# Optimization experiments

Measured on AMD Instinct MI355X. Metric: run time of the kernel, lower is better.

Reference implementation:

```python
import jax, jax.numpy as jnp
import numpy as np

B, S, D = 2, 2048, 1024
H, DK, DV = 16, 64, 64

def setup_inputs() -> dict:
    key = jax.random.key(0)
    ks = jax.random.split(key, 16)
    sc = 0.02
    inp = {
        'Q': jax.random.normal(ks[0], (B, S, D), jnp.float32),
        'K': jax.random.normal(ks[1], (B, S, D), jnp.float32),
        'V': jax.random.normal(ks[2], (B, S, D), jnp.float32),
        'attn_mask': jax.random.randint(ks[3], (B, S, S), 0, 2) > 0,
        'wq': jax.random.normal(ks[4], (H * DK, D), jnp.float32) * sc,
        'bq': jnp.zeros((H * DK,), jnp.float32),
        'wk': jax.random.normal(ks[5], (H * DK, D), jnp.float32) * sc,
        'bk': jnp.zeros((H * DK,), jnp.float32),
        'wv': jax.random.normal(ks[6], (H * DV, D), jnp.float32) * sc,
        'bv': jnp.zeros((H * DV,), jnp.float32),
        'wo': jax.random.normal(ks[7], (D, H * DV), jnp.float32) * sc,
        'bo': jnp.zeros((D,), jnp.float32),
        'gamma': jnp.ones((D,), jnp.float32),
        'beta': jnp.zeros((D,), jnp.float32),
    }
    return inp

def reference(Q, K, V, attn_mask, wq, bq, wk, bk, wv, bv, wo, bo, gamma, beta):
    b = Q.shape[0]
    # Faithful to torch: .view(B, H, -1, dk) with NO transpose (reshape-based head split)
    q = (Q @ wq.T + bq).reshape(b, H, -1, DK)
    k = (K @ wk.T + bk).reshape(b, H, -1, DK)
    v = (V @ wv.T + bv).reshape(b, H, -1, DV)
    scores = jnp.einsum('bhqd,bhkd->bhqk', q, k) / np.sqrt(DK).astype(np.float32)
    scores = jnp.where(attn_mask[:, None, :, :], jnp.float32(-1e9), scores)
    attn = jax.nn.softmax(scores, axis=-1)
    context = jnp.einsum('bhqk,bhkd->bhqd', attn, v)  # [B,H,S,dv]
    context = context.transpose(0, 2, 1, 3).reshape(b, -1, H * DV)
    output = context @ wo.T + bo
    x = output + Q
    mu = jnp.mean(x, axis=-1, keepdims=True)
    var = jnp.var(x, axis=-1, keepdims=True)
    return (x - mu) / jnp.sqrt(var + 1e-5) * gamma + beta
```

## Files before the change

### kernel.cpp

```cpp
#include <hip/hip_runtime.h>
#include <hip/hip_bf16.h>
#include <stdint.h>

typedef __bf16 bf16_t;
typedef __bf16 bf16x8 __attribute__((ext_vector_type(8)));
typedef __bf16 bf16x4 __attribute__((ext_vector_type(4)));
typedef float  f32x4  __attribute__((ext_vector_type(4)));

#if __has_builtin(__builtin_amdgcn_exp2f)
#define EXP2F __builtin_amdgcn_exp2f
#else
#define EXP2F exp2f
#endif


__device__ __forceinline__ void async_copy16(void* lds, const void* gptr) {
  __builtin_amdgcn_global_load_lds(
      (const __attribute__((address_space(1))) void*)gptr,
      (__attribute__((address_space(3))) void*)lds, 16, 0, 0);
}

__device__ __forceinline__ f32x4 splat4(float x) {
  f32x4 r; r[0] = x; r[1] = x; r[2] = x; r[3] = x; return r;
}

__device__ __forceinline__ uint32_t pack_bf16(float lo, float hi) {
  const uint32_t l = (uint32_t)__builtin_bit_cast(unsigned short, (bf16_t)lo);
  const uint32_t h = (uint32_t)__builtin_bit_cast(unsigned short, (bf16_t)hi);
  return (h << 16) | l;
}

__device__ __forceinline__ bool detect_fp32(const void* p) {
  const uint16_t* h = (const uint16_t*)p;
  int weird_even = 0, zero_even = 0, nz_odd = 0;
  for (int i = 0; i < 32; ++i) {
    uint16_t e = h[2 * i], o = h[2 * i + 1];
    int ee = (e >> 7) & 0xFF;
    if (e == 0) zero_even++;
    else if (ee < 90 || ee > 160) weird_even++;
    if (o != 0) nz_odd++;
  }
  return (weird_even >= 6) || (zero_even == 32 && nz_odd >= 1);
}

__global__ __launch_bounds__(256) void convert_all(
    const void* s0, const void* s1, const void* s2, const void* s3,
    const void* s4, const void* s5, const void* s6, const void* s7,
    const void* s8, const void* s9, const void* s10, const void* s11,
    const void* s12, char* __restrict__ ws) {
  const void* srcs[13] = {s0, s1, s2, s3, s4, s5, s6, s7, s8, s9, s10, s11, s12};
  const int counts[13] = {4194304, 4194304, 4194304,
                          1048576, 1024, 1048576, 1024,
                          1048576, 1024, 1048576, 1024,
                          1024, 1024};
  const size_t dofs[13] = {
      0ull, 8ull << 20, 16ull << 20,
      24ull << 20, (32ull << 20) + 0 * 8192, 26ull << 20, (32ull << 20) + 1 * 8192,
      28ull << 20, (32ull << 20) + 2 * 8192, 30ull << 20, (32ull << 20) + 3 * 8192,
      (32ull << 20) + 4 * 8192, (32ull << 20) + 5 * 8192};
  const int bi = blockIdx.y;
  const void* src = srcs[bi];
  bf16x8* dst = (bf16x8*)(ws + dofs[bi]);
  const int nv = counts[bi] >> 3;
  const bool f32 = detect_fp32(src);
  const int idx = blockIdx.x * 256 + threadIdx.x;
  const int stride = gridDim.x * 256;
  if (f32) {
    const float4* s4p = (const float4*)src;
    for (int i = idx; i < nv; i += stride) {
      float4 a = s4p[2 * i], b = s4p[2 * i + 1];
      bf16x8 o;
      o[0] = (bf16_t)a.x; o[1] = (bf16_t)a.y; o[2] = (bf16_t)a.z; o[3] = (bf16_t)a.w;
      o[4] = (bf16_t)b.x; o[5] = (bf16_t)b.y; o[6] = (bf16_t)b.z; o[7] = (bf16_t)b.w;
      dst[i] = o;
    }
  } else {
    const bf16x8* s8p = (const bf16x8*)src;
    for (int i = idx; i < nv; i += stride) dst[i] = s8p[i];
  }
}

__device__ __forceinline__ int detect_mask(const uint8_t* p) {
  const uint32_t* w = (const uint32_t*)p;
  bool i32 = true;
  for (int i = 0; i < 32; ++i) i32 &= (w[i] <= 1u);
  if (i32) return 0;
  const uint16_t* hh = (const uint16_t*)p;
  bool evz = true, oddok = true, allbf = true, allf16 = true;
  for (int i = 0; i < 32; ++i) {
    uint16_t e = hh[2 * i], o = hh[2 * i + 1];
    evz &= (e == 0);
    oddok &= (o == 0 || o == 0x3F80);
    allbf &= (e == 0 || e == 0x3F80) && (o == 0 || o == 0x3F80);
    allf16 &= (e == 0 || e == 0x3C00) && (o == 0 || o == 0x3C00);
  }
  if (evz && oddok) return 1;
  if (allbf || allf16) return 2;
  return 3;
}

__global__ __launch_bounds__(256) void mask_pack(const uint8_t* __restrict__ mraw,
                                                 uint8_t* __restrict__ outp) {
  const int mode = detect_mask(mraw);
  const int bq = blockIdx.x;
  const int L = threadIdx.x;
  uint32_t byte = 0;
  if (mode <= 1) {
    const uint4* m = (const uint4*)mraw;
    const size_t b4 = (size_t)bq * 512 + L * 2;
    uint4 a = m[b4], c = m[b4 + 1];
    byte = (a.x != 0u ? 1u : 0u) | (a.y != 0u ? 2u : 0u) |
           (a.z != 0u ? 4u : 0u) | (a.w != 0u ? 8u : 0u) |
           (c.x != 0u ? 16u : 0u) | (c.y != 0u ? 32u : 0u) |
           (c.z != 0u ? 64u : 0u) | (c.w != 0u ? 128u : 0u);
  } else if (mode == 2) {
    const uint16_t* m = (const uint16_t*)mraw;
    const size_t base = (size_t)bq * 2048 + L * 8;
    for (int j = 0; j < 8; ++j) byte |= (m[base + j] != 0 ? 1u : 0u) << j;
  } else {
    const size_t base = (size_t)bq * 2048 + L * 8;
    for (int j = 0; j < 8; ++j) byte |= (mraw[base + j] != 0 ? 1u : 0u) << j;
  }
  outp[(size_t)bq * 256 + L] = (uint8_t)byte;
}

template <int MODE, int BM>
__device__ __forceinline__ void gemm_tile(const bf16_t* __restrict__ X,
                                          const bf16_t* __restrict__ W,
                                          const bf16_t* __restrict__ bias,
                                          const float* __restrict__ QresF,
                                          const bf16_t* __restrict__ QresB,
                                          bool qres_is_f32,
                                          void* __restrict__ outv) {
  __shared__ __align__(16) bf16_t sA[BM * 32];
  __shared__ __align__(16) bf16_t sB[128 * 32];
  const int tm = blockIdx.x * BM;
  const int tn = blockIdx.y * 128;
  const int t = threadIdx.x;
  const int w = t >> 6, l = t & 63, lc = l & 15, ql = l >> 4;
  const int wm = (BM == 128) ? (w >> 1) * 64 : 0;
  const int wn = (BM == 128) ? (w & 1) * 64 : w * 32;
  const int NJ = (BM == 128) ? 4 : 2;
  f32x4 acc[4][(BM == 128) ? 4 : 2];
  for (int i = 0; i < 4; ++i)
    for (int j = 0; j < NJ; ++j) acc[i][j] = splat4(0.0f);

  const int m0 = t >> 2;
  const int kc0 = (t & 3) * 8;

  for (int k0 = 0; k0 < 1024; k0 += 32) {
    __syncthreads();
    async_copy16((char*)sA + w * 1024, X + (size_t)(tm + m0) * 1024 + k0 + kc0);
    if (BM == 128)
      async_copy16((char*)sA + 4096 + w * 1024,
                   X + (size_t)(tm + 64 + m0) * 1024 + k0 + kc0);
    async_copy16((char*)sB + w * 1024,        W + (size_t)(tn + m0) * 1024 + k0 + kc0);
    async_copy16((char*)sB + 4096 + w * 1024, W + (size_t)(tn + 64 + m0) * 1024 + k0 + kc0);
    __syncthreads();

    bf16x8 af[4], bfr[(BM == 128) ? 4 : 2];
    for (int i = 0; i < 4; ++i)
      af[i] = *(const bf16x8*)(sA + (wm + i * 16 + lc) * 32 + ql * 8);
    for (int j = 0; j < NJ; ++j)
      bfr[j] = *(const bf16x8*)(sB + (wn + j * 16 + lc) * 32 + ql * 8);
    for (int i = 0; i < 4; ++i)
      for (int j = 0; j < NJ; ++j)
        acc[i][j] = __builtin_amdgcn_mfma_f32_16x16x32_bf16(af[i], bfr[j], acc[i][j], 0, 0, 0);
  }

  float bvals[(BM == 128) ? 4 : 2];
  for (int j = 0; j < NJ; ++j) bvals[j] = (float)bias[tn + wn + j * 16 + lc];
  for (int i = 0; i < 4; ++i) {
    for (int j = 0; j < NJ; ++j) {
      const int col = tn + wn + j * 16 + lc;
      for (int v = 0; v < 4; ++v) {
        const int row = tm + wm + i * 16 + ql * 4 + v;
        float val = acc[i][j][v] + bvals[j];
        if (MODE == 0) {
          ((bf16_t*)outv)[(size_t)row * 1024 + col] = (bf16_t)val;
        } else if (MODE == 3) {
          ((bf16_t*)outv)[(size_t)row * 1024 + col] = (bf16_t)(val * 0.18033688f);
        } else if (MODE == 1) {
          const int b = row >> 11;
          const int x = (row & 2047) * 1024 + col;
          const int h = x >> 17;
          const int s = (x >> 6) & 2047;
          const int d = x & 63;
          ((bf16_t*)outv)[(size_t)((b * 16 + h) * 64 + d) * 2048 + s] = (bf16_t)val;
        } else {
          val += qres_is_f32 ? QresF[(size_t)row * 1024 + col]
                             : (float)QresB[(size_t)row * 1024 + col];
          ((float*)outv)[(size_t)row * 1024 + col] = val;
        }
      }
    }
  }
}

__global__ __launch_bounds__(256, 2) void qkv_gemm(
    const bf16_t* __restrict__ Q, const bf16_t* __restrict__ K, const bf16_t* __restrict__ V,
    const bf16_t* __restrict__ wq, const bf16_t* __restrict__ bq,
    const bf16_t* __restrict__ wk, const bf16_t* __restrict__ bk,
    const bf16_t* __restrict__ wv, const bf16_t* __restrict__ bv,
    bf16_t* __restrict__ qlin, bf16_t* __restrict__ klin, bf16_t* __restrict__ vT) {
  if (blockIdx.z == 0)      gemm_tile<3, 128>(Q, wq, bq, nullptr, nullptr, false, qlin);
  else if (blockIdx.z == 1) gemm_tile<0, 128>(K, wk, bk, nullptr, nullptr, false, klin);
  else                      gemm_tile<1, 128>(V, wv, bv, nullptr, nullptr, false, vT);
}

__global__ __launch_bounds__(256, 2) void final_gemm(
    const bf16_t* __restrict__ ctx, const bf16_t* __restrict__ wo,
    const bf16_t* __restrict__ bo, const bf16_t* __restrict__ QresB,
    const void* __restrict__ Qraw, float* __restrict__ xres) {
  const bool qf32 = detect_fp32(Qraw);
  gemm_tile<2, 64>(ctx, wo, bo, (const float*)Qraw, QresB, qf32, xres);
}

__global__ __launch_bounds__(512, 4) void attn(const bf16_t* __restrict__ qlin,
                                               const bf16_t* __restrict__ klin,
                                               const bf16_t* __restrict__ vT,
                                               const uint8_t* __restrict__ mQb,
                                               bf16_t* __restrict__ ctx) {
  __shared__ __align__(16) bf16_t sK[128 * 64];
  __shared__ __align__(16) bf16_t sVt[64 * 128];
  __shared__ __align__(16) uint8_t sM[128 * 16];

  const int t = threadIdx.x, w = t >> 6, l = t & 63, lc = l & 15, ql = l >> 4;
  const int bid = blockIdx.x;
  const int qt = (bid >> 3) & 15;
  const int combo = (bid & 7) * 4 + (bid >> 7);
  const int h = combo & 15, b = combo >> 4;
  const int q0 = qt * 128, rb = w * 16;

  const bf16_t* qh = qlin + (size_t)(b * 16 + h) * 2048 * 64;
  const bf16_t* kh = klin + (size_t)(b * 16 + h) * 2048 * 64;
  const bf16_t* vh = vT   + (size_t)(b * 16 + h) * 64 * 2048;
  const uint8_t* mh = mQb + ((size_t)(b * 2048 + q0)) * 256;

  const int kRow = t >> 3;
  const int kChk = (t & 7) ^ ((t >> 3) & 7);
  const int vRow = t >> 4;
  const int vChk = (t & 15) ^ ((t >> 4) & 15);

  bf16x8 qf[2];
  for (int c = 0; c < 2; ++c)
    qf[c] = *(const bf16x8*)(qh + (size_t)(q0 + rb + lc) * 64 + c * 32 + ql * 8);

  bf16x8 vones;
  for (int v = 0; v < 8; ++v) vones[v] = (bf16_t)1.0f;

  f32x4 oacc[4], osum = splat4(0.0f);
  for (int n = 0; n < 4; ++n) oacc[n] = splat4(0.0f);

  for (int kt = 0; kt < 16; ++kt) {
    const int k0 = kt * 128;
    __syncthreads();
    for (int is = 0; is < 2; ++is)
      async_copy16((char*)sK + is * 8192 + w * 1024,
                   kh + (size_t)(k0 + is * 64 + kRow) * 64 + kChk * 8);
    for (int is = 0; is < 2; ++is)
      async_copy16((char*)sVt + is * 8192 + w * 1024,
                   vh + (size_t)(is * 32 + vRow) * 2048 + k0 + vChk * 8);
    if (w < 2)
      async_copy16((char*)sM + w * 1024, mh + (size_t)(w * 64 + l) * 256 + kt * 16);
    __syncthreads();

    f32x4 sc[8];
#pragma unroll
    for (int j = 0; j < 8; ++j) {
      const char* kbase = (const char*)sK + (j * 16 + lc) * 128;
      bf16x8 ka0 = *(const bf16x8*)(kbase + ((ql    ) ^ (lc & 7)) * 16);
      bf16x8 ka1 = *(const bf16x8*)(kbase + ((ql + 4) ^ (lc & 7)) * 16);
      sc[j] = __builtin_amdgcn_mfma_f32_16x16x32_bf16(ka0, qf[0], splat4(0.0f), 0, 0, 0);
      sc[j] = __builtin_amdgcn_mfma_f32_16x16x32_bf16(ka1, qf[1], sc[j], 0, 0, 0);
    }

    const uint4 mq = *(const uint4*)(sM + (rb + lc) * 16);
    const int sh = ql << 2;
    const uint32_t ms[4] = {mq.x >> sh, mq.y >> sh, mq.z >> sh, mq.w >> sh};
    uint4 pq[4];
#pragma unroll
    for (int j = 0; j < 8; ++j) {
      const uint32_t m4 = (j & 1) ? (ms[j >> 1] >> 16) : ms[j >> 1];
      float e0 = EXP2F(sc[j][0]); e0 = (m4 & 1u) ? 0.0f : e0;
      float e1 = EXP2F(sc[j][1]); e1 = (m4 & 2u) ? 0.0f : e1;
      float e2 = EXP2F(sc[j][2]); e2 = (m4 & 4u) ? 0.0f : e2;
      float e3 = EXP2F(sc[j][3]); e3 = (m4 & 8u) ? 0.0f : e3;
      const uint32_t d01 = pack_bf16(e0, e1);
      const uint32_t d23 = pack_bf16(e2, e3);
      if ((j & 1) == 0) { pq[j >> 1].x = d01; pq[j >> 1].y = d23; }
      else              { pq[j >> 1].z = d01; pq[j >> 1].w = d23; }
    }

#pragma unroll
    for (int p = 0; p < 4; ++p) {
      const bf16x8 a0 = __builtin_bit_cast(bf16x8, pq[p]);
      osum = __builtin_amdgcn_mfma_f32_16x16x32_bf16(a0, vones, osum, 0, 0, 0);
#pragma unroll
      for (int n = 0; n < 4; ++n) {
        const char* vrow = (const char*)sVt + (n * 16 + lc) * 256 + (ql & 1) * 8;
        const uint2 lo = *(const uint2*)(vrow + (((4 * p     + (ql >> 1)) ^ lc) * 16));
        const uint2 hi = *(const uint2*)(vrow + (((4 * p + 2 + (ql >> 1)) ^ lc) * 16));
        const uint4 vbu = {lo.x, lo.y, hi.x, hi.y};
        const bf16x8 vb = __builtin_bit_cast(bf16x8, vbu);
        oacc[n] = __builtin_amdgcn_mfma_f32_16x16x32_bf16(a0, vb, oacc[n], 0, 0, 0);
      }
    }
  }

  f32x4 linv;
  for (int v = 0; v < 4; ++v) linv[v] = 1.0f / osum[v];
  for (int n = 0; n < 4; ++n) {
    f32x4 o = oacc[n] * linv;
    for (int v = 0; v < 4; ++v) {
      const int row = q0 + rb + ql * 4 + v;
      ctx[(size_t)(b * 2048 + row) * 1024 + h * 64 + n * 16 + lc] = (bf16_t)o[v];
    }
  }
}

__global__ __launch_bounds__(256) void ln_k(float* __restrict__ x,
                                            const bf16_t* __restrict__ gamma,
                                            const bf16_t* __restrict__ beta) {
  const int row = blockIdx.x, t = threadIdx.x, w = t >> 6, l = t & 63;
  float* xr = x + (size_t)row * 1024;
  float4 xv = ((const float4*)xr)[t];
  float v0 = xv.x, v1 = xv.y, v2 = xv.z, v3 = xv.w;
  float s1 = v0 + v1 + v2 + v3;
  float s2 = v0 * v0 + v1 * v1 + v2 * v2 + v3 * v3;
  for (int d = 1; d < 64; d <<= 1) {
    s1 += __shfl_xor(s1, d, 64);
    s2 += __shfl_xor(s2, d, 64);
  }
  __shared__ float red[8];
  if (l == 0) { red[w] = s1; red[4 + w] = s2; }
  __syncthreads();
  s1 = red[0] + red[1] + red[2] + red[3];
  s2 = red[4] + red[5] + red[6] + red[7];
  const float mean = s1 * (1.0f / 1024.0f);
  const float var = s2 * (1.0f / 1024.0f) - mean * mean;
  const float rstd = rsqrtf(var + 1e-5f);
  bf16x4 gv = *(const bf16x4*)(gamma + t * 4);
  bf16x4 bv = *(const bf16x4*)(beta + t * 4);
  float4 ov;
  ov.x = (v0 - mean) * rstd * (float)gv[0] + (float)bv[0];
  ov.y = (v1 - mean) * rstd * (float)gv[1] + (float)bv[1];
  ov.z = (v2 - mean) * rstd * (float)gv[2] + (float)bv[2];
  ov.w = (v3 - mean) * rstd * (float)gv[3] + (float)bv[3];
  ((float4*)xr)[t] = ov;
}

extern "C" void kernel_launch(void* const* d_in, const int* in_sizes, int n_in,
                              void* d_out, int out_size, void* d_ws, size_t ws_size,
                              hipStream_t stream) {
  const uint8_t* msk = (const uint8_t*)d_in[3];

  char* ws = (char*)d_ws;
  bf16_t* Qc   = (bf16_t*)(ws + 0);
  bf16_t* Kc   = (bf16_t*)(ws + (8ull << 20));
  bf16_t* Vc   = (bf16_t*)(ws + (16ull << 20));
  bf16_t* wqc  = (bf16_t*)(ws + (24ull << 20));
  bf16_t* wkc  = (bf16_t*)(ws + (26ull << 20));
  bf16_t* wvc  = (bf16_t*)(ws + (28ull << 20));
  bf16_t* woc  = (bf16_t*)(ws + (30ull << 20));
  bf16_t* bqc  = (bf16_t*)(ws + (32ull << 20) + 0 * 8192);
  bf16_t* bkc  = (bf16_t*)(ws + (32ull << 20) + 1 * 8192);
  bf16_t* bvc  = (bf16_t*)(ws + (32ull << 20) + 2 * 8192);
  bf16_t* boc  = (bf16_t*)(ws + (32ull << 20) + 3 * 8192);
  bf16_t* gc   = (bf16_t*)(ws + (32ull << 20) + 4 * 8192);
  bf16_t* bec  = (bf16_t*)(ws + (32ull << 20) + 5 * 8192);
  uint8_t* mQb = (uint8_t*)(ws + (33ull << 20));
  bf16_t* qlin = (bf16_t*)(ws + (34ull << 20));
  bf16_t* klin = (bf16_t*)(ws + (42ull << 20));
  bf16_t* vT   = (bf16_t*)(ws + (50ull << 20));
  bf16_t* ctx  = Kc;
  float* outF  = (float*)d_out;

  convert_all<<<dim3(512, 13), 256, 0, stream>>>(
      d_in[0], d_in[1], d_in[2], d_in[4], d_in[5], d_in[6], d_in[7],
      d_in[8], d_in[9], d_in[10], d_in[11], d_in[12], d_in[13], ws);
  mask_pack<<<dim3(4096), 256, 0, stream>>>(msk, mQb);
  qkv_gemm<<<dim3(32, 8, 3), 256, 0, stream>>>(Qc, Kc, Vc, wqc, bqc, wkc, bkc,
                                               wvc, bvc, qlin, klin, vT);
  attn<<<dim3(512), 512, 0, stream>>>(qlin, klin, vT, mQb, ctx);
  final_gemm<<<dim3(64, 8), 256, 0, stream>>>(ctx, woc, boc, nullptr, d_in[0], outF);
  ln_k<<<dim3(4096), 256, 0, stream>>>(outF, gc, bec);
}
```

Baseline: 307.7 us.

## Fuse Q/K/V projections into one block per tile and inline the output GEMM

The QKV GEMM now has each block compute the same output tile for all three projections, launching 256 blocks instead of 768. Each block holds 48 accumulator fragments per thread and about 40KB of LDS staging. The final GEMM is inlined with a 1D grid and its unused bf16 residual parameter removed. The intent is to cut block-launch and tail overhead, but register pressure triples and occupancy may drop, leaving fewer blocks to cover the CUs.

```diff
diff --git a/kernel.cpp b/kernel.cpp
--- a/kernel.cpp
+++ b/kernel.cpp
@@ -124,96 +124,145 @@
   outp[(size_t)bq * 256 + L] = (uint8_t)byte;
 }
 
-template <int MODE, int BM>
-__device__ __forceinline__ void gemm_tile(const bf16_t* __restrict__ X,
-                                          const bf16_t* __restrict__ W,
-                                          const bf16_t* __restrict__ bias,
-                                          const float* __restrict__ QresF,
-                                          const bf16_t* __restrict__ QresB,
-                                          bool qres_is_f32,
-                                          void* __restrict__ outv) {
-  __shared__ __align__(16) bf16_t sA[BM * 32];
-  __shared__ __align__(16) bf16_t sB[128 * 32];
-  const int tm = blockIdx.x * BM;
-  const int tn = blockIdx.y * 128;
-  const int t = threadIdx.x;
-  const int w = t >> 6, l = t & 63, lc = l & 15, ql = l >> 4;
-  const int wm = (BM == 128) ? (w >> 1) * 64 : 0;
-  const int wn = (BM == 128) ? (w & 1) * 64 : w * 32;
-  const int NJ = (BM == 128) ? 4 : 2;
-  f32x4 acc[4][(BM == 128) ? 4 : 2];
-  for (int i = 0; i < 4; ++i)
-    for (int j = 0; j < NJ; ++j) acc[i][j] = splat4(0.0f);
-
-  const int m0 = t >> 2;
-  const int kc0 = (t & 3) * 8;
-
-  for (int k0 = 0; k0 < 1024; k0 += 32) {
-    __syncthreads();
-    async_copy16((char*)sA + w * 1024, X + (size_t)(tm + m0) * 1024 + k0 + kc0);
-    if (BM == 128)
-      async_copy16((char*)sA + 4096 + w * 1024,
-                   X + (size_t)(tm + 64 + m0) * 1024 + k0 + kc0);
-    async_copy16((char*)sB + w * 1024,        W + (size_t)(tn + m0) * 1024 + k0 + kc0);
-    async_copy16((char*)sB + 4096 + w * 1024, W + (size_t)(tn + 64 + m0) * 1024 + k0 + kc0);
-    __syncthreads();
-
-    bf16x8 af[4], bfr[(BM == 128) ? 4 : 2];
-    for (int i = 0; i < 4; ++i)
-      af[i] = *(const bf16x8*)(sA + (wm + i * 16 + lc) * 32 + ql * 8);
-    for (int j = 0; j < NJ; ++j)
-      bfr[j] = *(const bf16x8*)(sB + (wn + j * 16 + lc) * 32 + ql * 8);
-    for (int i = 0; i < 4; ++i)
-      for (int j = 0; j < NJ; ++j)
-        acc[i][j] = __builtin_amdgcn_mfma_f32_16x16x32_bf16(af[i], bfr[j], acc[i][j], 0, 0, 0);
-  }
-
-  float bvals[(BM == 128) ? 4 : 2];
-  for (int j = 0; j < NJ; ++j) bvals[j] = (float)bias[tn + wn + j * 16 + lc];
-  for (int i = 0; i < 4; ++i) {
-    for (int j = 0; j < NJ; ++j) {
-      const int col = tn + wn + j * 16 + lc;
-      for (int v = 0; v < 4; ++v) {
-        const int row = tm + wm + i * 16 + ql * 4 + v;
-        float val = acc[i][j][v] + bvals[j];
-        if (MODE == 0) {
-          ((bf16_t*)outv)[(size_t)row * 1024 + col] = (bf16_t)val;
-        } else if (MODE == 3) {
-          ((bf16_t*)outv)[(size_t)row * 1024 + col] = (bf16_t)(val * 0.18033688f);
-        } else if (MODE == 1) {
-          const int b = row >> 11;
-          const int x = (row & 2047) * 1024 + col;
-          const int h = x >> 17;
-          const int s = (x >> 6) & 2047;
-          const int d = x & 63;
-          ((bf16_t*)outv)[(size_t)((b * 16 + h) * 64 + d) * 2048 + s] = (bf16_t)val;
-        } else {
-          val += qres_is_f32 ? QresF[(size_t)row * 1024 + col]
-                             : (float)QresB[(size_t)row * 1024 + col];
-          ((float*)outv)[(size_t)row * 1024 + col] = val;
-        }
-      }
-    }
-  }
-}
-
 __global__ __launch_bounds__(256, 2) void qkv_gemm(
-    const bf16_t* __restrict__ Q, const bf16_t* __restrict__ K, const bf16_t* __restrict__ V,
+    const bf16_t* __restrict__ Qc, const bf16_t* __restrict__ Kc,
+    const bf16_t* __restrict__ Vc,
     const bf16_t* __restrict__ wq, const bf16_t* __restrict__ bq,
     const bf16_t* __restrict__ wk, const bf16_t* __restrict__ bk,
     const bf16_t* __restrict__ wv, const bf16_t* __restrict__ bv,
     bf16_t* __restrict__ qlin, bf16_t* __restrict__ klin, bf16_t* __restrict__ vT) {
-  if (blockIdx.z == 0)      gemm_tile<3, 128>(Q, wq, bq, nullptr, nullptr, false, qlin);
-  else if (blockIdx.z == 1) gemm_tile<0, 128>(K, wk, bk, nullptr, nullptr, false, klin);
-  else                      gemm_tile<1, 128>(V, wv, bv, nullptr, nullptr, false, vT);
+  __shared__ __align__(16) bf16_t sA[3][64 * 32];
+  __shared__ __align__(16) bf16_t sB[3][128 * 32];
+  __shared__ __align__(16) bf16_t sA2[3][64 * 32];
+  const int bid = blockIdx.x;
+  const int tm = (bid >> 3) * 128;
+  const int tn = (bid & 7) * 128;
+  const int t = threadIdx.x;
+  const int w = t >> 6, l = t & 63, lc = l & 15, ql = l >> 4;
+  const int wm = (w >> 1) * 64, wn = (w & 1) * 64;
+  const bf16_t* As[3] = {Qc, Kc, Vc};
+  const bf16_t* Ws[3] = {wq, wk, wv};
+
+  f32x4 acc[3][4][4];
+  for (int s = 0; s < 3; ++s)
+    for (int i = 0; i < 4; ++i)
+      for (int j = 0; j < 4; ++j) acc[s][i][j] = splat4(0.0f);
+
+  const int m0 = t >> 2;
+  const int kc0 = (t & 3) * 8;
+
+  for (int k0 = 0; k0 < 1024; k0 += 32) {
+    __syncthreads();
+    for (int s = 0; s < 3; ++s) {
+      async_copy16((char*)sA[s] + w * 1024,
+                   As[s] + (size_t)(tm + m0) * 1024 + k0 + kc0);
+      async_copy16((char*)sA2[s] + w * 1024,
+                   As[s] + (size_t)(tm + 64 + m0) * 1024 + k0 + kc0);
+      async_copy16((char*)sB[s] + w * 1024,
+                   Ws[s] + (size_t)(tn + m0) * 1024 + k0 + kc0);
+      async_copy16((char*)sB[s] + 4096 + w * 1024,
+                   Ws[s] + (size_t)(tn + 64 + m0) * 1024 + k0 + kc0);
+    }
+    __syncthreads();
+
+    for (int s = 0; s < 3; ++s) {
+      const bf16_t* aBase = (wm == 0) ? sA[s] : sA2[s];
+      bf16x8 af[4], bfr[4];
+      for (int i = 0; i < 4; ++i)
+        af[i] = *(const bf16x8*)(aBase + (i * 16 + lc) * 32 + ql * 8);
+      for (int j = 0; j < 4; ++j)
+        bfr[j] = *(const bf16x8*)(sB[s] + (wn + j * 16 + lc) * 32 + ql * 8);
+      for (int i = 0; i < 4; ++i)
+        for (int j = 0; j < 4; ++j)
+          acc[s][i][j] =
+              __builtin_amdgcn_mfma_f32_16x16x32_bf16(af[i], bfr[j], acc[s][i][j], 0, 0, 0);
+    }
+  }
+
+  const bf16_t* Bs[3] = {bq, bk, bv};
+  for (int s = 0; s < 3; ++s) {
+    float bvals[4];
+    for (int j = 0; j < 4; ++j) bvals[j] = (float)Bs[s][tn + wn + j * 16 + lc];
+    for (int i = 0; i < 4; ++i) {
+      for (int j = 0; j < 4; ++j) {
+        const int col = tn + wn + j * 16 + lc;
+        for (int v = 0; v < 4; ++v) {
+          const int row = tm + wm + i * 16 + ql * 4 + v;
+          float val = acc[s][i][j][v] + bvals[j];
+          if (s == 0) {
+            qlin[(size_t)row * 1024 + col] = (bf16_t)(val * 0.18033688f);
+          } else if (s == 1) {
+            klin[(size_t)row * 1024 + col] = (bf16_t)val;
+          } else {
+            const int b = row >> 11;
+            const int x = (row & 2047) * 1024 + col;
+            const int h = x >> 17;
+            const int sq = (x >> 6) & 2047;
+            const int d = x & 63;
+            vT[(size_t)((b * 16 + h) * 64 + d) * 2048 + sq] = (bf16_t)val;
+          }
+        }
+      }
+    }
+  }
 }
 
 __global__ __launch_bounds__(256, 2) void final_gemm(
     const bf16_t* __restrict__ ctx, const bf16_t* __restrict__ wo,
-    const bf16_t* __restrict__ bo, const bf16_t* __restrict__ QresB,
-    const void* __restrict__ Qraw, float* __restrict__ xres) {
+    const bf16_t* __restrict__ bo, const void* __restrict__ Qraw,
+    float* __restrict__ xres) {
+  __shared__ __align__(16) bf16_t sA[64 * 32];
+  __shared__ __align__(16) bf16_t sB[128 * 32];
+  const int bid = blockIdx.x;
+  const int tm = (bid >> 3) * 64;
+  const int tn = (bid & 7) * 128;
+  const int t = threadIdx.x;
+  const int w = t >> 6, l = t & 63, lc = l & 15, ql = l >> 4;
+  const int wn = w * 32;
   const bool qf32 = detect_fp32(Qraw);
-  gemm_tile<2, 64>(ctx, wo, bo, (const float*)Qraw, QresB, qf32, xres);
+  const float* QresF = (const float*)Qraw;
+  const bf16_t* QresB = (const bf16_t*)Qraw;
+
+  f32x4 acc[4][2];
+  for (int i = 0; i < 4; ++i)
+    for (int j = 0; j < 2; ++j) acc[i][j] = splat4(0.0f);
+
+  const int m0 = t >> 2;
+  const int kc0 = (t & 3) * 8;
+
+  for (int k0 = 0; k0 < 1024; k0 += 32) {
+    __syncthreads();
+    if (w < 1)
+      ;
+    async_copy16((char*)sA + w * 1024, ctx + (size_t)(tm + m0 / 1) * 1024 + k0 + kc0);
+    async_copy16((char*)sB + w * 1024,        wo + (size_t)(tn + m0) * 1024 + k0 + kc0);
+    async_copy16((char*)sB + 4096 + w * 1024, wo + (size_t)(tn + 64 + m0) * 1024 + k0 + kc0);
+    __syncthreads();
+
+    bf16x8 af[4], bfr[2];
+    for (int i = 0; i < 4; ++i)
+      af[i] = *(const bf16x8*)(sA + (i * 16 + lc) * 32 + ql * 8);
+    for (int j = 0; j < 2; ++j)
+      bfr[j] = *(const bf16x8*)(sB + (wn + j * 16 + lc) * 32 + ql * 8);
+    for (int i = 0; i < 4; ++i)
+      for (int j = 0; j < 2; ++j)
+        acc[i][j] = __builtin_amdgcn_mfma_f32_16x16x32_bf16(af[i], bfr[j], acc[i][j], 0, 0, 0);
+  }
+
+  float bvals[2];
+  for (int j = 0; j < 2; ++j) bvals[j] = (float)bo[tn + wn + j * 16 + lc];
+  for (int i = 0; i < 4; ++i) {
+    for (int j = 0; j < 2; ++j) {
+      const int col = tn + wn + j * 16 + lc;
+      for (int v = 0; v < 4; ++v) {
+        const int row = tm + i * 16 + ql * 4 + v;
+        float val = acc[i][j][v] + bvals[j];
+        val += qf32 ? QresF[(size_t)row * 1024 + col]
+                    : (float)QresB[(size_t)row * 1024 + col];
+        xres[(size_t)row * 1024 + col] = val;
+      }
+    }
+  }
 }
 
 __global__ __launch_bounds__(512, 4) void attn(const bf16_t* __restrict__ qlin,
@@ -380,9 +429,9 @@
       d_in[0], d_in[1], d_in[2], d_in[4], d_in[5], d_in[6], d_in[7],
       d_in[8], d_in[9], d_in[10], d_in[11], d_in[12], d_in[13], ws);
   mask_pack<<<dim3(4096), 256, 0, stream>>>(msk, mQb);
-  qkv_gemm<<<dim3(32, 8, 3), 256, 0, stream>>>(Qc, Kc, Vc, wqc, bqc, wkc, bkc,
-                                               wvc, bvc, qlin, klin, vT);
+  qkv_gemm<<<dim3(256), 256, 0, stream>>>(Qc, Kc, Vc, wqc, bqc, wkc, bkc,
+                                          wvc, bvc, qlin, klin, vT);
   attn<<<dim3(512), 512, 0, stream>>>(qlin, klin, vT, mQb, ctx);
-  final_gemm<<<dim3(64, 8), 256, 0, stream>>>(ctx, woc, boc, nullptr, d_in[0], outF);
+  final_gemm<<<dim3(512), 256, 0, stream>>>(ctx, woc, boc, d_in[0], outF);
   ln_k<<<dim3(4096), 256, 0, stream>>>(outF, gc, bec);
 }
```

New measurement: 339.6 us. 10.4% more time.
